# Kernel tuning notes

Hardware: AMD Instinct MI355X
Metric: run time of the kernel (lower is better)

## Reference

```python
import jax, jax.numpy as jnp
import numpy as np

D_MODEL = 1024
NUM_HEADS = 16
DEPTH = D_MODEL // NUM_HEADS


def setup_inputs() -> dict:
    key = jax.random.key(0)
    ks = jax.random.split(key, 11)
    B, S = 2, 2048
    scale = 1.0 / np.sqrt(D_MODEL)
    inp = {
        "q": jax.random.normal(ks[0], (B, S, D_MODEL), dtype=jnp.float32),
        "k": jax.random.normal(ks[1], (B, S, D_MODEL), dtype=jnp.float32),
        "v": jax.random.normal(ks[2], (B, S, D_MODEL), dtype=jnp.float32),
        "mask": jnp.zeros((B, 1, 1, S), dtype=jnp.float32),
        "wq": jax.random.normal(ks[3], (D_MODEL, D_MODEL), dtype=jnp.float32) * scale,
        "bq": jnp.zeros((D_MODEL,), dtype=jnp.float32),
        "wk": jax.random.normal(ks[4], (D_MODEL, D_MODEL), dtype=jnp.float32) * scale,
        "bk": jnp.zeros((D_MODEL,), dtype=jnp.float32),
        "wv": jax.random.normal(ks[5], (D_MODEL, D_MODEL), dtype=jnp.float32) * scale,
        "bv": jnp.zeros((D_MODEL,), dtype=jnp.float32),
        "wo": jax.random.normal(ks[6], (D_MODEL, D_MODEL), dtype=jnp.float32) * scale,
        "bo": jnp.zeros((D_MODEL,), dtype=jnp.float32),
    }
    return inp


def _split_heads(x):
    # [B, S, D] -> [B, H, S, depth]
    B, S, _ = x.shape
    return x.reshape(B, S, NUM_HEADS, DEPTH).transpose(0, 2, 1, 3)


def reference(q, k, v, mask, wq, bq, wk, bk, wv, bv, wo, bo):
    B, S, _ = q.shape
    qh = _split_heads(q @ wq + bq)  # [B,H,S,d]
    kh = _split_heads(k @ wk + bk)
    vh = _split_heads(v @ wv + bv)
    logits = jnp.einsum("bhsd,bhtd->bhst", qh, kh) / jnp.sqrt(
        jnp.asarray(DEPTH, dtype=qh.dtype)
    )
    logits = logits + mask * -1e9
    attn = jax.nn.softmax(logits, axis=-1)  # [B,H,S,S]
    ctx = jnp.einsum("bhst,bhtd->bhsd", attn, vh)
    ctx = ctx.transpose(0, 2, 1, 3).reshape(B, S, D_MODEL)
    out = ctx @ wo + bo
    return out, attn
```

## Files before the change

kernel.cpp:

```cpp
#include <hip/hip_runtime.h>
#include <cstdint>
#include <cstddef>

typedef __bf16 bf16;
typedef __attribute__((ext_vector_type(8))) __bf16 bf16x8;
typedef __attribute__((ext_vector_type(4))) __bf16 bf16x4;
typedef __attribute__((ext_vector_type(4))) float f32x4;

#define DM 1024
#define NH 16
#define DEPTH 64
#define SEQ 2048
#define NB 2

__device__ __forceinline__ void split2(float x, bf16& h, bf16& l) {
    h = (bf16)x;
    l = (bf16)(x - (float)h);
}

__device__ __forceinline__ f32x4 mfma16(bf16x8 a, bf16x8 b, f32x4 c) {
    return __builtin_amdgcn_mfma_f32_16x16x32_bf16(a, b, c, 0, 0, 0);
}

__device__ __forceinline__ void gload16(const bf16* g, bf16* s) {
    __builtin_amdgcn_global_load_lds(
        (const __attribute__((address_space(1))) void*)g,
        (__attribute__((address_space(3))) void*)s, 16, 0, 0);
}

__global__ __launch_bounds__(256) void split_kernel(const float* __restrict__ x,
                                                    bf16* __restrict__ hi,
                                                    bf16* __restrict__ lo, int n) {
    int i = (blockIdx.x * 256 + threadIdx.x) * 4;
    if (i >= n) return;
    float4 v = *(const float4*)(x + i);
    bf16 h0, l0, h1, l1, h2, l2, h3, l3;
    split2(v.x, h0, l0); split2(v.y, h1, l1);
    split2(v.z, h2, l2); split2(v.w, h3, l3);
    bf16x4 hv = {h0, h1, h2, h3}, lv = {l0, l1, l2, l3};
    *(bf16x4*)(hi + i) = hv;
    *(bf16x4*)(lo + i) = lv;
}

__global__ __launch_bounds__(256) void wsplit_t(const float* __restrict__ w,
                                                bf16* __restrict__ hi,
                                                bf16* __restrict__ lo) {
    __shared__ float tile[64][65];
    int t = threadIdx.x;
    int c0 = blockIdx.x * 64;
    int r0 = blockIdx.y * 64;
    int r = t >> 2, cg = (t & 3) * 16;
#pragma unroll
    for (int j = 0; j < 16; j += 4) {
        float4 v = *(const float4*)(w + (size_t)(r0 + r) * DM + c0 + cg + j);
        tile[r][cg + j] = v.x; tile[r][cg + j + 1] = v.y;
        tile[r][cg + j + 2] = v.z; tile[r][cg + j + 3] = v.w;
    }
    __syncthreads();
    int n = t >> 2, kg = (t & 3) * 16;
    bf16x8 hv0, hv1, lv0, lv1;
#pragma unroll
    for (int i = 0; i < 8; i++) {
        bf16 h, l;
        split2(tile[kg + i][n], h, l); hv0[i] = h; lv0[i] = l;
        split2(tile[kg + 8 + i][n], h, l); hv1[i] = h; lv1[i] = l;
    }
    size_t o = (size_t)(c0 + n) * DM + r0 + kg;
    *(bf16x8*)(hi + o) = hv0; *(bf16x8*)(hi + o + 8) = hv1;
    *(bf16x8*)(lo + o) = lv0; *(bf16x8*)(lo + o + 8) = lv1;
}

__global__ __launch_bounds__(512) void gemm_split(
    const bf16* __restrict__ Ah, const bf16* __restrict__ Al,
    const bf16* __restrict__ Bh, const bf16* __restrict__ Bl,
    const float* __restrict__ bias,
    bf16* __restrict__ Ch, bf16* __restrict__ Cl, float* __restrict__ Cf) {
    __shared__ bf16 lds4[2][4][128 * 64];
    int t = threadIdx.x;
    int m0 = blockIdx.x * 128, n0 = blockIdx.y * 128;
    int l = t & 63, w = t >> 6;
    int quad = l >> 4, ln = l & 15;
    int wr = w >> 2, wc = w & 3;
    int rch = l >> 3, c16 = l & 7;
    int sx0 = (quad ^ (ln & 7)) << 3;

    int bufid = w >> 1;
    const bf16* src = (bufid == 0) ? Ah : (bufid == 1) ? Al : (bufid == 2) ? Bh : Bl;
    int rbase = (bufid < 2) ? m0 : n0;
    int ch0 = (w & 1) * 8;

    auto stage = [&](int db, int k0) {
#pragma unroll
        for (int j = 0; j < 8; j++) {
            int chunk = ch0 + j;
            int row = chunk * 8 + rch;
            gload16(src + (size_t)(rbase + row) * DM + k0 + ((c16 ^ (row & 7)) << 3),
                    &lds4[db][bufid][chunk * 512]);
        }
    };

    f32x4 acc[4][2];
#pragma unroll
    for (int r = 0; r < 4; r++)
#pragma unroll
        for (int c = 0; c < 2; c++) acc[r][c] = (f32x4){0.f, 0.f, 0.f, 0.f};

    stage(0, 0);
    __syncthreads();

    for (int kk = 0; kk < DM / 64; kk++) {
        int cur = kk & 1;
        if (kk < DM / 64 - 1) stage(cur ^ 1, (kk + 1) * 64);
#pragma unroll
        for (int k2 = 0; k2 < 2; k2++) {
            int so = sx0 ^ (k2 << 5);
            bf16x8 ah[4], al[4], bh[2], bl[2];
#pragma unroll
            for (int r = 0; r < 4; r++) {
                int ro = (wr * 64 + r * 16 + ln) << 6;
                ah[r] = *(const bf16x8*)&lds4[cur][0][ro + so];
                al[r] = *(const bf16x8*)&lds4[cur][1][ro + so];
            }
#pragma unroll
            for (int c = 0; c < 2; c++) {
                int ro = (wc * 32 + c * 16 + ln) << 6;
                bh[c] = *(const bf16x8*)&lds4[cur][2][ro + so];
                bl[c] = *(const bf16x8*)&lds4[cur][3][ro + so];
            }
#pragma unroll
            for (int r = 0; r < 4; r++)
#pragma unroll
                for (int c = 0; c < 2; c++) {
                    acc[r][c] = mfma16(ah[r], bh[c], acc[r][c]);
                    acc[r][c] = mfma16(ah[r], bl[c], acc[r][c]);
                    acc[r][c] = mfma16(al[r], bh[c], acc[r][c]);
                }
        }
        __syncthreads();
    }

#pragma unroll
    for (int c = 0; c < 2; c++) {
        int col = n0 + wc * 32 + c * 16 + ln;
        float bv = bias[col];
#pragma unroll
        for (int r = 0; r < 4; r++) {
            int rowb = m0 + wr * 64 + r * 16 + quad * 4;
#pragma unroll
            for (int i = 0; i < 4; i++) {
                float v = acc[r][c][i] + bv;
                size_t o = (size_t)(rowb + i) * DM + col;
                if (Cf) {
                    Cf[o] = v;
                } else {
                    bf16 h, lo_;
                    split2(v, h, lo_);
                    Ch[o] = h; Cl[o] = lo_;
                }
            }
        }
    }
}

__global__ __launch_bounds__(256) void vtrans(const bf16* __restrict__ vh_h,
                                              const bf16* __restrict__ vh_l,
                                              bf16* __restrict__ vt_h,
                                              bf16* __restrict__ vt_l) {
    __shared__ bf16 tile[64][72];
    int t = threadIdx.x;
    int s0 = blockIdx.x * 64;
    int bh = blockIdx.y;
    int b = bh >> 4, h = bh & 15;
    const bf16* src[2] = {vh_h, vh_l};
    bf16* dst[2] = {vt_h, vt_l};
#pragma unroll
    for (int p = 0; p < 2; p++) {
#pragma unroll
        for (int rnd = 0; rnd < 2; rnd++) {
            int unit = t + rnd * 256;
            int r = unit >> 3, cg = (unit & 7) * 8;
            *(bf16x8*)&tile[r][cg] =
                *(const bf16x8*)(src[p] + (size_t)(b * SEQ + s0 + r) * DM + h * DEPTH + cg);
        }
        __syncthreads();
#pragma unroll
        for (int rnd = 0; rnd < 2; rnd++) {
            int unit = t + rnd * 256;
            int d = unit >> 3, sg = (unit & 7) * 8;
            bf16x8 v;
#pragma unroll
            for (int j = 0; j < 8; j++) v[j] = tile[sg + j][d];
            *(bf16x8*)(dst[p] + (size_t)(bh * DEPTH + d) * SEQ + s0 + sg) = v;
        }
        __syncthreads();
    }
}

#define PST 76
__global__ __launch_bounds__(512) void attn_kernel(
    const bf16* __restrict__ qh_h, const bf16* __restrict__ qh_l,
    const bf16* __restrict__ kh_h, const bf16* __restrict__ kh_l,
    const bf16* __restrict__ vt_h, const bf16* __restrict__ vt_l,
    const float* __restrict__ mask,
    float* __restrict__ attn, bf16* __restrict__ ctx_h, bf16* __restrict__ ctx_l) {
    __shared__ bf16 lK[2][2][64 * 64];
    __shared__ bf16 lV[2][2][64 * 64];
    __shared__ bf16 lPh[128 * PST], lPl[128 * PST];
    int t = threadIdx.x;
    int m0 = blockIdx.x * 128;
    int bh = blockIdx.y;
    int b = bh >> 4, h = bh & 15;
    int l = t & 63, w = t >> 6, quad = l >> 4, ln = l & 15;
    int rch = l >> 3, c16 = l & 7;
    int sx0 = (quad ^ (ln & 7)) << 3;

    bf16x8 qf_h[2], qf_l[2];
    {
        size_t qrow = (size_t)(b * SEQ + m0 + w * 16 + ln) * DM + h * DEPTH;
#pragma unroll
        for (int kk = 0; kk < 2; kk++) {
            qf_h[kk] = *(const bf16x8*)(qh_h + qrow + kk * 32 + quad * 8);
            qf_l[kk] = *(const bf16x8*)(qh_l + qrow + kk * 32 + quad * 8);
        }
    }

    const bf16* ksrc1 = (w < 4) ? kh_h : kh_l;
    int kbuf1 = (w < 4) ? 0 : 1;
    int kch0 = (w & 3) * 2;
    auto stageK = [&](int db, int t0) {
#pragma unroll
        for (int j = 0; j < 2; j++) {
            int chunk = kch0 + j;
            int row = chunk * 8 + rch;
            gload16(ksrc1 + (size_t)(b * SEQ + t0 + row) * DM + h * DEPTH +
                        ((c16 ^ (row & 7)) << 3),
                    &lK[db][kbuf1][chunk * 512]);
        }
    };
    int tgt = w >> 1;
    const bf16* ksrc2 = (tgt == 0) ? kh_h : (tgt == 1) ? kh_l : (tgt == 2) ? vt_h : vt_l;
    auto stageKV = [&](int db, int t0) {
        bf16* dst = (tgt == 0) ? &lK[db][0][0] : (tgt == 1) ? &lK[db][1][0]
                  : (tgt == 2) ? &lV[db][0][0] : &lV[db][1][0];
#pragma unroll
        for (int j = 0; j < 4; j++) {
            int chunk = (w & 1) * 4 + j;
            int row = chunk * 8 + rch;
            size_t off = (tgt >= 2)
                             ? ((size_t)(bh * DEPTH + row) * SEQ + t0)
                             : ((size_t)(b * SEQ + t0 + row) * DM + h * DEPTH);
            gload16(ksrc2 + off + ((c16 ^ (row & 7)) << 3), dst + chunk * 512);
        }
    };

    float rowsum[4] = {0.f, 0.f, 0.f, 0.f};
    stageK(0, 0);
    __syncthreads();
    for (int ct = 0; ct < SEQ / 64; ct++) {
        int db = ct & 1;
        if (ct < SEQ / 64 - 1) stageK(db ^ 1, (ct + 1) * 64);
        int t0 = ct * 64;
#pragma unroll
        for (int c = 0; c < 4; c++) {
            f32x4 s = (f32x4){0.f, 0.f, 0.f, 0.f};
#pragma unroll
            for (int kk = 0; kk < 2; kk++) {
                int so = sx0 ^ (kk << 5);
                int ro = (c * 16 + ln) << 6;
                bf16x8 kb_h = *(const bf16x8*)&lK[db][0][ro + so];
                bf16x8 kb_l = *(const bf16x8*)&lK[db][1][ro + so];
                s = mfma16(qf_h[kk], kb_h, s);
                s = mfma16(qf_h[kk], kb_l, s);
                s = mfma16(qf_l[kk], kb_h, s);
            }
            int col = t0 + c * 16 + ln;
            float mv = mask[b * SEQ + col] * -1e9f;
#pragma unroll
            for (int i = 0; i < 4; i++) rowsum[i] += __expf(s[i] * 0.125f + mv);
        }
        __syncthreads();
    }
#pragma unroll
    for (int m = 1; m < 16; m <<= 1)
#pragma unroll
        for (int i = 0; i < 4; i++) rowsum[i] += __shfl_xor(rowsum[i], m, 64);
    float linv[4];
#pragma unroll
    for (int i = 0; i < 4; i++) linv[i] = 1.0f / rowsum[i];

    f32x4 o[4];
#pragma unroll
    for (int c2 = 0; c2 < 4; c2++) o[c2] = (f32x4){0.f, 0.f, 0.f, 0.f};

    stageKV(0, 0);
    __syncthreads();
    for (int ct = 0; ct < SEQ / 64; ct++) {
        int db = ct & 1;
        if (ct < SEQ / 64 - 1) stageKV(db ^ 1, (ct + 1) * 64);
        int t0 = ct * 64;
#pragma unroll
        for (int c = 0; c < 4; c++) {
            f32x4 s = (f32x4){0.f, 0.f, 0.f, 0.f};
#pragma unroll
            for (int kk = 0; kk < 2; kk++) {
                int so = sx0 ^ (kk << 5);
                int ro = (c * 16 + ln) << 6;
                bf16x8 kb_h = *(const bf16x8*)&lK[db][0][ro + so];
                bf16x8 kb_l = *(const bf16x8*)&lK[db][1][ro + so];
                s = mfma16(qf_h[kk], kb_h, s);
                s = mfma16(qf_h[kk], kb_l, s);
                s = mfma16(qf_l[kk], kb_h, s);
            }
            int col = t0 + c * 16 + ln;
            float mv = mask[b * SEQ + col] * -1e9f;
#pragma unroll
            for (int i = 0; i < 4; i++) {
                float p = __expf(s[i] * 0.125f + mv) * linv[i];
                __builtin_nontemporal_store(
                    p, attn + ((size_t)bh * SEQ + m0 + w * 16 + quad * 4 + i) * SEQ + col);
                bf16 ph, pl;
                split2(p, ph, pl);
                int pr = (w * 16 + quad * 4 + i) * PST + c * 16 + ln;
                lPh[pr] = ph;
                lPl[pr] = pl;
            }
        }
#pragma unroll
        for (int kk = 0; kk < 2; kk++) {
            int so = sx0 ^ (kk << 5);
            bf16x8 pa_h = *(const bf16x8*)&lPh[(w * 16 + ln) * PST + kk * 32 + quad * 8];
            bf16x8 pa_l = *(const bf16x8*)&lPl[(w * 16 + ln) * PST + kk * 32 + quad * 8];
#pragma unroll
            for (int c2 = 0; c2 < 4; c2++) {
                int ro = (c2 * 16 + ln) << 6;
                bf16x8 vb_h = *(const bf16x8*)&lV[db][0][ro + so];
                bf16x8 vb_l = *(const bf16x8*)&lV[db][1][ro + so];
                o[c2] = mfma16(pa_h, vb_h, o[c2]);
                o[c2] = mfma16(pa_h, vb_l, o[c2]);
                o[c2] = mfma16(pa_l, vb_h, o[c2]);
            }
        }
        __syncthreads();
    }

#pragma unroll
    for (int c2 = 0; c2 < 4; c2++) {
        int d = c2 * 16 + ln;
#pragma unroll
        for (int i = 0; i < 4; i++) {
            int row = m0 + w * 16 + quad * 4 + i;
            bf16 hh, ll;
            split2(o[c2][i], hh, ll);
            size_t oo = (size_t)(b * SEQ + row) * DM + h * DEPTH + d;
            ctx_h[oo] = hh; ctx_l[oo] = ll;
        }
    }
}

extern "C" void kernel_launch(void* const* d_in, const int* in_sizes, int n_in,
                              void* d_out, int out_size, void* d_ws, size_t ws_size,
                              hipStream_t stream) {
    (void)in_sizes; (void)n_in; (void)out_size; (void)ws_size;
    const float* q    = (const float*)d_in[0];
    const float* k    = (const float*)d_in[1];
    const float* v    = (const float*)d_in[2];
    const float* mask = (const float*)d_in[3];
    const float* wq   = (const float*)d_in[4];
    const float* bq   = (const float*)d_in[5];
    const float* wk   = (const float*)d_in[6];
    const float* bk   = (const float*)d_in[7];
    const float* wv   = (const float*)d_in[8];
    const float* bv   = (const float*)d_in[9];
    const float* wo   = (const float*)d_in[10];
    const float* bo   = (const float*)d_in[11];

    float* out  = (float*)d_out;
    float* attn = out + (size_t)NB * SEQ * DM;

    const size_t E  = (size_t)NB * SEQ * DM;
    const size_t WE = (size_t)DM * DM;

    bf16* p = (bf16*)d_ws;
    bf16* q_h = p;            bf16* q_l = q_h + E;
    bf16* k_h = q_l + E;      bf16* k_l = k_h + E;
    bf16* v_h = k_l + E;      bf16* v_l = v_h + E;
    bf16* wqT_h = v_l + E;    bf16* wqT_l = wqT_h + WE;
    bf16* wkT_h = wqT_l + WE; bf16* wkT_l = wkT_h + WE;
    bf16* wvT_h = wkT_l + WE; bf16* wvT_l = wvT_h + WE;
    bf16* woT_h = wvT_l + WE; bf16* woT_l = woT_h + WE;
    bf16* qh_h = woT_l + WE;  bf16* qh_l = qh_h + E;
    bf16* kh_h = qh_l + E;    bf16* kh_l = kh_h + E;
    bf16* vh_h = kh_l + E;    bf16* vh_l = vh_h + E;
    bf16* vt_h = q_h;  bf16* vt_l = q_l;
    bf16* ctx_h = k_h; bf16* ctx_l = k_l;

    dim3 blk(256);
    split_kernel<<<(int)(E / 1024), blk, 0, stream>>>(q, q_h, q_l, (int)E);
    split_kernel<<<(int)(E / 1024), blk, 0, stream>>>(k, k_h, k_l, (int)E);
    split_kernel<<<(int)(E / 1024), blk, 0, stream>>>(v, v_h, v_l, (int)E);
    wsplit_t<<<dim3(16, 16), blk, 0, stream>>>(wq, wqT_h, wqT_l);
    wsplit_t<<<dim3(16, 16), blk, 0, stream>>>(wk, wkT_h, wkT_l);
    wsplit_t<<<dim3(16, 16), blk, 0, stream>>>(wv, wvT_h, wvT_l);
    wsplit_t<<<dim3(16, 16), blk, 0, stream>>>(wo, woT_h, woT_l);

    gemm_split<<<dim3(32, 8), dim3(512), 0, stream>>>(q_h, q_l, wqT_h, wqT_l, bq, qh_h, qh_l, nullptr);
    gemm_split<<<dim3(32, 8), dim3(512), 0, stream>>>(k_h, k_l, wkT_h, wkT_l, bk, kh_h, kh_l, nullptr);
    gemm_split<<<dim3(32, 8), dim3(512), 0, stream>>>(v_h, v_l, wvT_h, wvT_l, bv, vh_h, vh_l, nullptr);

    vtrans<<<dim3(32, 32), blk, 0, stream>>>(vh_h, vh_l, vt_h, vt_l);

    attn_kernel<<<dim3(16, 32), dim3(512), 0, stream>>>(qh_h, qh_l, kh_h, kh_l, vt_h, vt_l,
                                                        mask, attn, ctx_h, ctx_l);

    gemm_split<<<dim3(32, 8), dim3(512), 0, stream>>>(ctx_h, ctx_l, woT_h, woT_l, bo,
                                                      nullptr, nullptr, out);
}
```

Measured before the change: 898.8 us.

## Deepen GEMM/attention pipelines, batch split kernels, cache mask in LDS

The GEMM moves from a 2-stage, 64-wide K pipeline to a 4-stage, 32-wide one, with a new XOR swizzle, explicit vmcnt waits and raw barriers in place of __syncthreads. The attention first pass gets a 4-deep K buffer with partial vmcnt waits. A precomputed mask is cached in LDS, and MFMA sections are wrapped in s_setprio. The three input split launches and four weight split launches are each merged into one launch, and the final output uses nontemporal stores. The aim is to hide global-load latency and cut launch and mask-load overhead, at the cost of more LDS per block (which may lower occupancy) and fragile hand-written waitcnt logic.

```diff
diff --git a/kernel.cpp b/kernel.cpp
--- a/kernel.cpp
+++ b/kernel.cpp
@@ -13,6 +13,9 @@
 #define SEQ 2048
 #define NB 2
 
+#define WAIT_LGKM0() asm volatile("s_waitcnt lgkmcnt(0)" ::: "memory")
+#define BAR() __builtin_amdgcn_s_barrier()
+
 __device__ __forceinline__ void split2(float x, bf16& h, bf16& l) {
     h = (bf16)x;
     l = (bf16)(x - (float)h);
@@ -28,24 +31,34 @@
         (__attribute__((address_space(3))) void*)s, 16, 0, 0);
 }
 
-__global__ __launch_bounds__(256) void split_kernel(const float* __restrict__ x,
-                                                    bf16* __restrict__ hi,
-                                                    bf16* __restrict__ lo, int n) {
+__global__ __launch_bounds__(256) void split3(
+    const float* __restrict__ q, const float* __restrict__ k, const float* __restrict__ v,
+    bf16* __restrict__ qh, bf16* __restrict__ ql, bf16* __restrict__ kh,
+    bf16* __restrict__ kl, bf16* __restrict__ vh, bf16* __restrict__ vl, int n) {
+    const float* x = blockIdx.y == 0 ? q : blockIdx.y == 1 ? k : v;
+    bf16* hi = blockIdx.y == 0 ? qh : blockIdx.y == 1 ? kh : vh;
+    bf16* lo = blockIdx.y == 0 ? ql : blockIdx.y == 1 ? kl : vl;
     int i = (blockIdx.x * 256 + threadIdx.x) * 4;
     if (i >= n) return;
-    float4 v = *(const float4*)(x + i);
+    float4 vv = *(const float4*)(x + i);
     bf16 h0, l0, h1, l1, h2, l2, h3, l3;
-    split2(v.x, h0, l0); split2(v.y, h1, l1);
-    split2(v.z, h2, l2); split2(v.w, h3, l3);
+    split2(vv.x, h0, l0); split2(vv.y, h1, l1);
+    split2(vv.z, h2, l2); split2(vv.w, h3, l3);
     bf16x4 hv = {h0, h1, h2, h3}, lv = {l0, l1, l2, l3};
     *(bf16x4*)(hi + i) = hv;
     *(bf16x4*)(lo + i) = lv;
 }
 
-__global__ __launch_bounds__(256) void wsplit_t(const float* __restrict__ w,
-                                                bf16* __restrict__ hi,
-                                                bf16* __restrict__ lo) {
+__global__ __launch_bounds__(256) void wsplit4(
+    const float* __restrict__ w0, const float* __restrict__ w1,
+    const float* __restrict__ w2, const float* __restrict__ w3,
+    bf16* __restrict__ h0, bf16* __restrict__ h1, bf16* __restrict__ h2, bf16* __restrict__ h3,
+    bf16* __restrict__ l0, bf16* __restrict__ l1, bf16* __restrict__ l2, bf16* __restrict__ l3) {
     __shared__ float tile[64][65];
+    int z = blockIdx.z;
+    const float* w = z == 0 ? w0 : z == 1 ? w1 : z == 2 ? w2 : w3;
+    bf16* hi = z == 0 ? h0 : z == 1 ? h1 : z == 2 ? h2 : h3;
+    bf16* lo = z == 0 ? l0 : z == 1 ? l1 : z == 2 ? l2 : l3;
     int t = threadIdx.x;
     int c0 = blockIdx.x * 64;
     int r0 = blockIdx.y * 64;
@@ -75,27 +88,26 @@
     const bf16* __restrict__ Bh, const bf16* __restrict__ Bl,
     const float* __restrict__ bias,
     bf16* __restrict__ Ch, bf16* __restrict__ Cl, float* __restrict__ Cf) {
-    __shared__ bf16 lds4[2][4][128 * 64];
+    __shared__ bf16 lds4[4][4][128 * 32];
     int t = threadIdx.x;
     int m0 = blockIdx.x * 128, n0 = blockIdx.y * 128;
     int l = t & 63, w = t >> 6;
     int quad = l >> 4, ln = l & 15;
     int wr = w >> 2, wc = w & 3;
-    int rch = l >> 3, c16 = l & 7;
-    int sx0 = (quad ^ (ln & 7)) << 3;
-
-    int bufid = w >> 1;
-    const bf16* src = (bufid == 0) ? Ah : (bufid == 1) ? Al : (bufid == 2) ? Bh : Bl;
-    int rbase = (bufid < 2) ? m0 : n0;
-    int ch0 = (w & 1) * 8;
+
+    int half = w & 1;
+    int arr = w >> 1;
+    const bf16* src = (arr == 0) ? Ah : (arr == 1) ? Al : (arr == 2) ? Bh : Bl;
+    int rbase = (arr < 2) ? m0 : n0;
 
     auto stage = [&](int db, int k0) {
 #pragma unroll
-        for (int j = 0; j < 8; j++) {
-            int chunk = ch0 + j;
-            int row = chunk * 8 + rch;
-            gload16(src + (size_t)(rbase + row) * DM + k0 + ((c16 ^ (row & 7)) << 3),
-                    &lds4[db][bufid][chunk * 512]);
+        for (int j = 0; j < 4; j++) {
+            int u = half * 256 + j * 64 + l;
+            int row = u >> 2;
+            int q = (u & 3) ^ (row & 3) ^ ((row >> 2) & 3);
+            gload16(src + (size_t)(rbase + row) * DM + k0 + q * 8,
+                    &lds4[db][arr][(half * 256 + j * 64) * 8]);
         }
     };
 
@@ -105,38 +117,45 @@
 #pragma unroll
         for (int c = 0; c < 2; c++) acc[r][c] = (f32x4){0.f, 0.f, 0.f, 0.f};
 
-    stage(0, 0);
-    __syncthreads();
-
-    for (int kk = 0; kk < DM / 64; kk++) {
-        int cur = kk & 1;
-        if (kk < DM / 64 - 1) stage(cur ^ 1, (kk + 1) * 64);
-#pragma unroll
-        for (int k2 = 0; k2 < 2; k2++) {
-            int so = sx0 ^ (k2 << 5);
-            bf16x8 ah[4], al[4], bh[2], bl[2];
-#pragma unroll
-            for (int r = 0; r < 4; r++) {
-                int ro = (wr * 64 + r * 16 + ln) << 6;
-                ah[r] = *(const bf16x8*)&lds4[cur][0][ro + so];
-                al[r] = *(const bf16x8*)&lds4[cur][1][ro + so];
-            }
+    stage(0, 0); stage(1, 32); stage(2, 64);
+    asm volatile("s_waitcnt vmcnt(8)" ::: "memory");
+    BAR();
+
+    for (int kk = 0; kk < 32; kk++) {
+        int cur = kk & 3;
+        if (kk + 3 < 32) stage((kk + 3) & 3, (kk + 3) * 32);
+
+        bf16x8 ah[4], al[4], bh2[2], bl2[2];
+#pragma unroll
+        for (int r = 0; r < 4; r++) {
+            int R = wr * 64 + r * 16 + ln;
+            int off = (R << 5) + ((quad ^ (R & 3) ^ ((R >> 2) & 3)) << 3);
+            ah[r] = *(const bf16x8*)&lds4[cur][0][off];
+            al[r] = *(const bf16x8*)&lds4[cur][1][off];
+        }
+#pragma unroll
+        for (int c = 0; c < 2; c++) {
+            int R = wc * 32 + c * 16 + ln;
+            int off = (R << 5) + ((quad ^ (R & 3) ^ ((R >> 2) & 3)) << 3);
+            bh2[c] = *(const bf16x8*)&lds4[cur][2][off];
+            bl2[c] = *(const bf16x8*)&lds4[cur][3][off];
+        }
+        __builtin_amdgcn_s_setprio(1);
+#pragma unroll
+        for (int r = 0; r < 4; r++)
 #pragma unroll
             for (int c = 0; c < 2; c++) {
-                int ro = (wc * 32 + c * 16 + ln) << 6;
-                bh[c] = *(const bf16x8*)&lds4[cur][2][ro + so];
-                bl[c] = *(const bf16x8*)&lds4[cur][3][ro + so];
-            }
-#pragma unroll
-            for (int r = 0; r < 4; r++)
-#pragma unroll
-                for (int c = 0; c < 2; c++) {
-                    acc[r][c] = mfma16(ah[r], bh[c], acc[r][c]);
-                    acc[r][c] = mfma16(ah[r], bl[c], acc[r][c]);
-                    acc[r][c] = mfma16(al[r], bh[c], acc[r][c]);
-                }
-        }
-        __syncthreads();
+                acc[r][c] = mfma16(ah[r], bh2[c], acc[r][c]);
+                acc[r][c] = mfma16(ah[r], bl2[c], acc[r][c]);
+                acc[r][c] = mfma16(al[r], bh2[c], acc[r][c]);
+            }
+        __builtin_amdgcn_s_setprio(0);
+
+        WAIT_LGKM0();
+        if (kk + 3 < 32)      asm volatile("s_waitcnt vmcnt(8)" ::: "memory");
+        else if (kk + 2 < 32) asm volatile("s_waitcnt vmcnt(4)" ::: "memory");
+        else                  asm volatile("s_waitcnt vmcnt(0)" ::: "memory");
+        BAR();
     }
 
 #pragma unroll
@@ -151,7 +170,7 @@
                 float v = acc[r][c][i] + bv;
                 size_t o = (size_t)(rowb + i) * DM + col;
                 if (Cf) {
-                    Cf[o] = v;
+                    __builtin_nontemporal_store(v, Cf + o);
                 } else {
                     bf16 h, lo_;
                     split2(v, h, lo_);
@@ -196,16 +215,17 @@
     }
 }
 
-#define PST 76
+#define PST 68
 __global__ __launch_bounds__(512) void attn_kernel(
     const bf16* __restrict__ qh_h, const bf16* __restrict__ qh_l,
     const bf16* __restrict__ kh_h, const bf16* __restrict__ kh_l,
     const bf16* __restrict__ vt_h, const bf16* __restrict__ vt_l,
     const float* __restrict__ mask,
     float* __restrict__ attn, bf16* __restrict__ ctx_h, bf16* __restrict__ ctx_l) {
-    __shared__ bf16 lK[2][2][64 * 64];
+    __shared__ bf16 lK[4][2][64 * 64];
     __shared__ bf16 lV[2][2][64 * 64];
     __shared__ bf16 lPh[128 * PST], lPl[128 * PST];
+    __shared__ float lM[SEQ];
     int t = threadIdx.x;
     int m0 = blockIdx.x * 128;
     int bh = blockIdx.y;
@@ -224,6 +244,14 @@
         }
     }
 
+    {
+        float4 mv4 = *(const float4*)(mask + b * SEQ + t * 4);
+        lM[t * 4 + 0] = mv4.x * -1e9f;
+        lM[t * 4 + 1] = mv4.y * -1e9f;
+        lM[t * 4 + 2] = mv4.z * -1e9f;
+        lM[t * 4 + 3] = mv4.w * -1e9f;
+    }
+
     const bf16* ksrc1 = (w < 4) ? kh_h : kh_l;
     int kbuf1 = (w < 4) ? 0 : 1;
     int kch0 = (w & 3) * 2;
@@ -254,31 +282,41 @@
     };
 
     float rowsum[4] = {0.f, 0.f, 0.f, 0.f};
-    stageK(0, 0);
-    __syncthreads();
+    stageK(0, 0); stageK(1, 64); stageK(2, 128);
+    asm volatile("s_waitcnt vmcnt(4) lgkmcnt(0)" ::: "memory");
+    BAR();
     for (int ct = 0; ct < SEQ / 64; ct++) {
-        int db = ct & 1;
-        if (ct < SEQ / 64 - 1) stageK(db ^ 1, (ct + 1) * 64);
+        int cur = ct & 3;
+        if (ct + 3 < SEQ / 64) stageK((ct + 3) & 3, (ct + 3) * 64);
         int t0 = ct * 64;
 #pragma unroll
         for (int c = 0; c < 4; c++) {
             f32x4 s = (f32x4){0.f, 0.f, 0.f, 0.f};
+            bf16x8 kb_h[2], kb_l[2];
 #pragma unroll
             for (int kk = 0; kk < 2; kk++) {
                 int so = sx0 ^ (kk << 5);
                 int ro = (c * 16 + ln) << 6;
-                bf16x8 kb_h = *(const bf16x8*)&lK[db][0][ro + so];
-                bf16x8 kb_l = *(const bf16x8*)&lK[db][1][ro + so];
-                s = mfma16(qf_h[kk], kb_h, s);
-                s = mfma16(qf_h[kk], kb_l, s);
-                s = mfma16(qf_l[kk], kb_h, s);
-            }
-            int col = t0 + c * 16 + ln;
-            float mv = mask[b * SEQ + col] * -1e9f;
+                kb_h[kk] = *(const bf16x8*)&lK[cur][0][ro + so];
+                kb_l[kk] = *(const bf16x8*)&lK[cur][1][ro + so];
+            }
+            __builtin_amdgcn_s_setprio(1);
+#pragma unroll
+            for (int kk = 0; kk < 2; kk++) {
+                s = mfma16(qf_h[kk], kb_h[kk], s);
+                s = mfma16(qf_h[kk], kb_l[kk], s);
+                s = mfma16(qf_l[kk], kb_h[kk], s);
+            }
+            __builtin_amdgcn_s_setprio(0);
+            float mv = lM[t0 + c * 16 + ln];
 #pragma unroll
             for (int i = 0; i < 4; i++) rowsum[i] += __expf(s[i] * 0.125f + mv);
         }
-        __syncthreads();
+        WAIT_LGKM0();
+        if (ct + 3 < SEQ / 64)      asm volatile("s_waitcnt vmcnt(4)" ::: "memory");
+        else if (ct + 2 < SEQ / 64) asm volatile("s_waitcnt vmcnt(2)" ::: "memory");
+        else                        asm volatile("s_waitcnt vmcnt(0)" ::: "memory");
+        BAR();
     }
 #pragma unroll
     for (int m = 1; m < 16; m <<= 1)
@@ -301,18 +339,24 @@
 #pragma unroll
         for (int c = 0; c < 4; c++) {
             f32x4 s = (f32x4){0.f, 0.f, 0.f, 0.f};
+            bf16x8 kb_h[2], kb_l[2];
 #pragma unroll
             for (int kk = 0; kk < 2; kk++) {
                 int so = sx0 ^ (kk << 5);
                 int ro = (c * 16 + ln) << 6;
-                bf16x8 kb_h = *(const bf16x8*)&lK[db][0][ro + so];
-                bf16x8 kb_l = *(const bf16x8*)&lK[db][1][ro + so];
-                s = mfma16(qf_h[kk], kb_h, s);
-                s = mfma16(qf_h[kk], kb_l, s);
-                s = mfma16(qf_l[kk], kb_h, s);
-            }
+                kb_h[kk] = *(const bf16x8*)&lK[db][0][ro + so];
+                kb_l[kk] = *(const bf16x8*)&lK[db][1][ro + so];
+            }
+            __builtin_amdgcn_s_setprio(1);
+#pragma unroll
+            for (int kk = 0; kk < 2; kk++) {
+                s = mfma16(qf_h[kk], kb_h[kk], s);
+                s = mfma16(qf_h[kk], kb_l[kk], s);
+                s = mfma16(qf_l[kk], kb_h[kk], s);
+            }
+            __builtin_amdgcn_s_setprio(0);
             int col = t0 + c * 16 + ln;
-            float mv = mask[b * SEQ + col] * -1e9f;
+            float mv = lM[col];
 #pragma unroll
             for (int i = 0; i < 4; i++) {
                 float p = __expf(s[i] * 0.125f + mv) * linv[i];
@@ -330,6 +374,7 @@
             int so = sx0 ^ (kk << 5);
             bf16x8 pa_h = *(const bf16x8*)&lPh[(w * 16 + ln) * PST + kk * 32 + quad * 8];
             bf16x8 pa_l = *(const bf16x8*)&lPl[(w * 16 + ln) * PST + kk * 32 + quad * 8];
+            __builtin_amdgcn_s_setprio(1);
 #pragma unroll
             for (int c2 = 0; c2 < 4; c2++) {
                 int ro = (c2 * 16 + ln) << 6;
@@ -339,6 +384,7 @@
                 o[c2] = mfma16(pa_h, vb_l, o[c2]);
                 o[c2] = mfma16(pa_l, vb_h, o[c2]);
             }
+            __builtin_amdgcn_s_setprio(0);
         }
         __syncthreads();
     }
@@ -395,13 +441,11 @@
     bf16* ctx_h = k_h; bf16* ctx_l = k_l;
 
     dim3 blk(256);
-    split_kernel<<<(int)(E / 1024), blk, 0, stream>>>(q, q_h, q_l, (int)E);
-    split_kernel<<<(int)(E / 1024), blk, 0, stream>>>(k, k_h, k_l, (int)E);
-    split_kernel<<<(int)(E / 1024), blk, 0, stream>>>(v, v_h, v_l, (int)E);
-    wsplit_t<<<dim3(16, 16), blk, 0, stream>>>(wq, wqT_h, wqT_l);
-    wsplit_t<<<dim3(16, 16), blk, 0, stream>>>(wk, wkT_h, wkT_l);
-    wsplit_t<<<dim3(16, 16), blk, 0, stream>>>(wv, wvT_h, wvT_l);
-    wsplit_t<<<dim3(16, 16), blk, 0, stream>>>(wo, woT_h, woT_l);
+    split3<<<dim3((int)(E / 1024), 3), blk, 0, stream>>>(q, k, v, q_h, q_l, k_h, k_l,
+                                                         v_h, v_l, (int)E);
+    wsplit4<<<dim3(16, 16, 4), blk, 0, stream>>>(wq, wk, wv, wo,
+                                                 wqT_h, wkT_h, wvT_h, woT_h,
+                                                 wqT_l, wkT_l, wvT_l, woT_l);
 
     gemm_split<<<dim3(32, 8), dim3(512), 0, stream>>>(q_h, q_l, wqT_h, wqT_l, bq, qh_h, qh_l, nullptr);
     gemm_split<<<dim3(32, 8), dim3(512), 0, stream>>>(k_h, k_l, wkT_h, wkT_l, bk, kh_h, kh_l, nullptr);
```

New measurement: 918.4 us. +2.2%, slower.
